# Kernel optimization log

Hardware: AMD Instinct MI355X
Metric: run time of the kernel (lower is better)

## Reference

```python
import jax, jax.numpy as jnp
import numpy as np

B, C, H8, W8 = 2, 256, 56, 96
RADIUS, LEVELS = 4, 4


def setup_inputs() -> dict:
    key = jax.random.key(0)
    k1, k2, k3, k4, k5 = jax.random.split(key, 5)
    fmap1 = jax.random.normal(k1, (B, C, H8, W8), jnp.float32)
    fmap2 = jax.random.normal(k2, (B, C, H8, W8), jnp.float32)
    xs = jnp.arange(W8, dtype=jnp.float32)
    ys = jnp.arange(H8, dtype=jnp.float32)
    bx, by = jnp.broadcast_arrays(xs[None, :], ys[:, None])
    base = jnp.stack([bx, by], axis=0)  # [2,H8,W8], x first (as create_coords_grid)
    coords = base[None] + 4.0 * jax.random.normal(k3, (B, 2, H8, W8), jnp.float32)
    flow = jax.random.normal(k4, (B, 2, H8, W8), jnp.float32)
    mask = jax.random.normal(k5, (B, 9 * 8 * 8, H8, W8), jnp.float32)
    return {"fmap1": fmap1, "fmap2": fmap2, "coords": coords, "flow": flow, "mask": mask}


def _bilinear_sample(cflat, Hl, Wl, px, py):
    # cflat: [N, Hl*Wl]; px,py: [N,P] pixel coords; zero padding outside (grid_sample default)
    x0 = jnp.floor(px)
    y0 = jnp.floor(py)
    wx = px - x0
    wy = py - y0
    x0 = x0.astype(jnp.int32)
    y0 = y0.astype(jnp.int32)

    def g(xi, yi):
        valid = (xi >= 0) & (xi <= Wl - 1) & (yi >= 0) & (yi <= Hl - 1)
        idx = jnp.clip(yi, 0, Hl - 1) * Wl + jnp.clip(xi, 0, Wl - 1)
        return jnp.where(valid, jnp.take_along_axis(cflat, idx, axis=1), 0.0)

    return ((1 - wy) * ((1 - wx) * g(x0, y0) + wx * g(x0 + 1, y0))
            + wy * ((1 - wx) * g(x0, y0 + 1) + wx * g(x0 + 1, y0 + 1)))


def _corr_lookup(fmap1, fmap2, coords):
    b, c, h, w = fmap1.shape
    n = b * h * w
    # all-pairs correlation, scaled by sqrt(C)
    corr = jnp.einsum('bchw,bcij->bhwij', fmap1, fmap2) / jnp.sqrt(jnp.float32(c))
    cl = corr.reshape(n, h, w)
    # query coords (pixel units at level 0)
    cx = coords[:, 0].reshape(n)
    cy = coords[:, 1].reshape(n)
    r = RADIUS
    lin = jnp.linspace(-r, r, 2 * r + 1, dtype=jnp.float32)
    # replicates torch.meshgrid(dy,dx) quirk: x-offset varies along axis 0, y along axis 1
    xo = jnp.repeat(lin, 2 * r + 1)  # [81]
    yo = jnp.tile(lin, 2 * r + 1)    # [81]
    outs = []
    for i in range(LEVELS):
        Hl, Wl = cl.shape[1], cl.shape[2]
        cflat = cl.reshape(n, Hl * Wl)
        px = cx[:, None] / (2 ** i) + xo[None, :]
        py = cy[:, None] / (2 ** i) + yo[None, :]
        samp = _bilinear_sample(cflat, Hl, Wl, px, py)  # [N,81]
        outs.append(samp.reshape(b, h, w, -1))
        if i < LEVELS - 1:  # 2x2 avg pool, stride 2
            cl = cl.reshape(n, Hl // 2, 2, Wl // 2, 2).mean(axis=(2, 4))
    out = jnp.concatenate(outs, axis=-1)  # [B,h,w,4*81]
    return out.transpose(0, 3, 1, 2)


def _convex_upsample(flow, mask):
    b, ch, h, w = flow.shape
    m = mask.reshape(b, 1, 9, 8, 8, h, w)
    m = jax.nn.softmax(m, axis=2)
    fp = jnp.pad(8.0 * flow, ((0, 0), (0, 0), (1, 1), (1, 1)))
    # 3x3 unfold, kernel positions row-major (matches F.unfold ordering)
    patches = jnp.stack([fp[:, :, i:i + h, j:j + w]
                         for i in range(3) for j in range(3)], axis=2)  # [B,2,9,h,w]
    up = jnp.sum(m * patches[:, :, :, None, None], axis=2)  # [B,2,8,8,h,w]
    up = up.transpose(0, 1, 4, 2, 5, 3)  # [B,2,h,8,w,8]
    return up.reshape(b, ch, 8 * h, 8 * w)


def reference(fmap1, fmap2, coords, flow, mask):
    corr_feats = _corr_lookup(fmap1, fmap2, coords)  # [B,324,H8,W8]
    up_flow = _convex_upsample(flow, mask)           # [B,2,8*H8,8*W8]
    return (corr_feats, up_flow)
```

## Files before the change

kernel.cpp:

```cpp
#include <hip/hip_runtime.h>
#include <math.h>

constexpr int B = 2, C = 256, H = 56, W = 96;
constexpr int HW = H * W;
constexpr int RADIUS = 4;

#define SQ 21.166666f
constexpr float SCL = 36.0f / (127.0f * 127.0f * 16.0f);

constexpr size_t F1T_B = 0;
constexpr size_t L0_B  = (size_t)B * HW * C;
constexpr size_t L1_B  = L0_B + (size_t)B * HW * C;
constexpr size_t L2_B  = L1_B + (size_t)B * 28 * 48 * C;
constexpr size_t L3_B  = L2_B + (size_t)B * 14 * 24 * C;
constexpr size_t OUT0_ELEMS = (size_t)B * 324 * HW;

static __device__ __forceinline__ int dot4acc(int a, int b, int c) {
#if __has_builtin(__builtin_amdgcn_sdot4)
    return __builtin_amdgcn_sdot4(a, b, c, false);
#else
    c += (int)(char)(a) * (int)(char)(b);
    c += (int)(char)(a >> 8) * (int)(char)(b >> 8);
    c += (int)(char)(a >> 16) * (int)(char)(b >> 16);
    c += (int)(char)(a >> 24) * (int)(char)(b >> 24);
    return c;
#endif
}

static __device__ __forceinline__ unsigned short pack_i8x2(float a, float b) {
    int ia = (int)rintf(a); ia = ia < -127 ? -127 : (ia > 127 ? 127 : ia);
    int ib = (int)rintf(b); ib = ib < -127 ? -127 : (ib > 127 ? 127 : ib);
    return (unsigned short)((ia & 0xFF) | ((ib & 0xFF) << 8));
}

constexpr int TP_BLOCKS = (HW / 32) * (C / 64) * 2 * B;
constexpr int CU_BLOCKS = B * H * 8;
constexpr int PL_BLOCKS = B * 7 * 12;
__global__ __launch_bounds__(256) void prep_kernel(
    const float* __restrict__ fmap1, const float* __restrict__ fmap2,
    const float* __restrict__ flow, const float* __restrict__ mask,
    char* __restrict__ ws, float* __restrict__ out1) {
    __shared__ float smem[72 * 96 + 2 * 3 * 98];
    int bid = blockIdx.x;
    int tid = threadIdx.x;

    if (bid < TP_BLOCKS) {
        float (*tile)[33] = (float(*)[33])smem;
        int zi = bid / 672;
        int rem = bid % 672;
        int by = rem / 168, bx = rem % 168;
        int b = zi & 1, m = zi >> 1;
        const float* src = m ? fmap2 : fmap1;
        unsigned short* dst = (unsigned short*)(ws + (m ? L0_B : F1T_B));
        int c0 = by * 64, q0 = bx * 32;
        int tx = tid & 31, ty = tid >> 5;
#pragma unroll
        for (int r = 0; r < 8; ++r) {
            int cl = ty + r * 8;
            tile[cl][tx] = src[((size_t)(b * C + c0 + cl)) * HW + q0 + tx];
        }
        __syncthreads();
#pragma unroll
        for (int r = 0; r < 4; ++r) {
            int pl = ty + r * 8;
            dst[((size_t)b * HW + q0 + pl) * 128 + (c0 >> 1) + tx] =
                pack_i8x2(tile[2 * tx][pl] * SQ, tile[2 * tx + 1][pl] * SQ);
        }
        return;
    }

    if (bid < TP_BLOCKS + CU_BLOCKS) {
        float* msk = smem;
        float* fst = smem + 72 * 96;
        int cb = bid - TP_BLOCKS;
        int i = cb & 7;
        int r = cb >> 3;
        int h = r % H;
        int b = r / H;

        for (int idx = tid; idx < 72 * 96; idx += 256) {
            int row = idx / 96, wc = idx - row * 96;
            int k = row >> 3, j = row & 7;
            int gl = k * 64 + i * 8 + j;
            msk[idx] = mask[((size_t)(b * 576 + gl)) * HW + h * W + wc];
        }
        for (int idx = tid; idx < 588; idx += 256) {
            int ch = idx / 294;
            int rem2 = idx - ch * 294;
            int rr = rem2 / 98;
            int xw = rem2 - rr * 98;
            int hh = h + rr - 1, ww = xw - 1;
            float v = 0.f;
            if (hh >= 0 && hh < H && ww >= 0 && ww < W)
                v = 8.0f * flow[((size_t)(b * 2 + ch)) * HW + hh * W + ww];
            fst[idx] = v;
        }
        __syncthreads();

#pragma unroll
        for (int rr = 0; rr < 3; ++rr) {
            int col = tid + rr * 256;
            int w = col >> 3, j = col & 7;
            float m[9], mx = -1e30f;
#pragma unroll
            for (int k = 0; k < 9; ++k) {
                m[k] = msk[(k * 8 + j) * 96 + w];
                mx = fmaxf(mx, m[k]);
            }
            float sum = 0.f;
#pragma unroll
            for (int k = 0; k < 9; ++k) {
                m[k] = __expf(m[k] - mx);
                sum += m[k];
            }
            float inv = 1.0f / sum;
            float a0 = 0.f, a1 = 0.f;
#pragma unroll
            for (int k = 0; k < 9; ++k) {
                int ki = k / 3, kj = k - ki * 3;
                float wgt = m[k] * inv;
                a0 = fmaf(wgt, fst[0 * 294 + ki * 98 + w + kj], a0);
                a1 = fmaf(wgt, fst[1 * 294 + ki * 98 + w + kj], a1);
            }
            size_t row8 = (size_t)8 * h + i;
            out1[((size_t)(b * 2 + 0) * 448 + row8) * 768 + col] = a0;
            out1[((size_t)(b * 2 + 1) * 448 + row8) * 768 + col] = a1;
        }
        return;
    }

    {
        int pb = bid - TP_BLOCKS - CU_BLOCKS;
        int b = pb / 84;
        int t = pb % 84;
        int y3 = t / 12, x3 = t % 12;
        int wv = tid >> 6, lane = tid & 63;
        int py = lane >> 3, px = lane & 7;

        unsigned short* D1 = (unsigned short*)(ws + L1_B);
        unsigned short* D2 = (unsigned short*)(ws + L2_B);
        unsigned short* D3 = (unsigned short*)(ws + L3_B);
        const float* srcp = fmap2 + (size_t)b * C * HW + (size_t)(y3 * 8 + py) * W + x3 * 8 + px;

        for (int j = wv * 32; j < wv * 32 + 32; ++j) {
            float va = srcp[(size_t)(2 * j) * HW];
            float vb = srcp[(size_t)(2 * j + 1) * HW];
            float a1 = va + __shfl_xor(va, 1); a1 += __shfl_xor(a1, 8);
            float b1 = vb + __shfl_xor(vb, 1); b1 += __shfl_xor(b1, 8);
            float a2 = a1 + __shfl_xor(a1, 2); a2 += __shfl_xor(a2, 16);
            float b2 = b1 + __shfl_xor(b1, 2); b2 += __shfl_xor(b2, 16);
            float a3 = a2 + __shfl_xor(a2, 4); a3 += __shfl_xor(a3, 32);
            float b3 = b2 + __shfl_xor(b2, 4); b3 += __shfl_xor(b3, 32);
            if ((lane & 9) == 0) {
                int Y = y3 * 4 + (py >> 1), X = x3 * 4 + (px >> 1);
                D1[((size_t)(b * 28 + Y) * 48 + X) * 128 + j] =
                    pack_i8x2(a1 * 0.25f * SQ, b1 * 0.25f * SQ);
            }
            if ((lane & 27) == 0) {
                int Y = y3 * 2 + (py >> 2), X = x3 * 2 + (px >> 2);
                D2[((size_t)(b * 14 + Y) * 24 + X) * 128 + j] =
                    pack_i8x2(a2 * 0.0625f * SQ, b2 * 0.0625f * SQ);
            }
            if (lane == 0) {
                D3[((size_t)(b * 7 + y3) * 12 + x3) * 128 + j] =
                    pack_i8x2(a3 * 0.015625f * SQ, b3 * 0.015625f * SQ);
            }
        }
    }
}

__global__ __launch_bounds__(256, 5) void corr_fused(
    const float* __restrict__ coords, const char* __restrict__ ws,
    float* __restrict__ out0) {
    __shared__ float Dsh[4][8][101];
    __shared__ float Wxy[4][8][2];

    int tid = threadIdx.x;
    int l = tid >> 6;
    int lane = tid & 63;
    int v = lane & 3;
    int grp = lane >> 2;

    int g0 = blockIdx.x * 8;
    int b = g0 / HW;
    int hw0 = g0 - b * HW;

    int Hl = H >> l, Wl = W >> l;
    size_t off = (l == 0 ? L0_B : (l == 1 ? L1_B : (l == 2 ? L2_B : L3_B)));
    const char* base8 = ws + off + (size_t)b * Hl * Wl * C;
    float scale = (l == 0 ? 1.0f : (l == 1 ? 0.5f : (l == 2 ? 0.25f : 0.125f)));

    int xo0 = grp < 10 ? grp : grp - 10;
    int yo0 = grp < 10 ? 0 : 1;

    const char* f1b = ws + F1T_B;

#pragma unroll 1
    for (int qi = 0; qi < 8; ++qi) {
        int g = g0 + qi;
        const int4* ap = (const int4*)(f1b + (size_t)g * C + (v << 6));
        int4 A0 = ap[0], A1 = ap[1], A2 = ap[2], A3 = ap[3];

        float cx = coords[(size_t)(b * 2 + 0) * HW + hw0 + qi];
        float cy = coords[(size_t)(b * 2 + 1) * HW + hw0 + qi];
        float fx = cx * scale, fy = cy * scale;
        float fxf = floorf(fx), fyf = floorf(fy);
        float wx = fx - fxf, wy = fy - fyf;
        int ix = (int)fxf, iy = (int)fyf;
        if (lane == 0) { Wxy[l][qi][0] = wx; Wxy[l][qi][1] = wy; }

        int xo = xo0, yo = yo0;
#pragma unroll
        for (int it = 0; it < 7; ++it) {
            bool live = (it < 6) | (grp < 4);
            int x = ix - RADIUS + xo;
            int y = iy - RADIUS + yo;
            int s0 = 0, s1 = 0, s2 = 0, s3 = 0;
            if (live && (unsigned)x < (unsigned)Wl && (unsigned)y < (unsigned)Hl) {
                const int4* cp = (const int4*)(base8 + ((y * Wl + x) << 8) + (v << 6));
                int4 c0 = cp[0], c1 = cp[1], c2 = cp[2], c3 = cp[3];
                s0 = dot4acc(c0.x, A0.x, s0); s1 = dot4acc(c0.y, A0.y, s1);
                s2 = dot4acc(c0.z, A0.z, s2); s3 = dot4acc(c0.w, A0.w, s3);
                s0 = dot4acc(c1.x, A1.x, s0); s1 = dot4acc(c1.y, A1.y, s1);
                s2 = dot4acc(c1.z, A1.z, s2); s3 = dot4acc(c1.w, A1.w, s3);
                s0 = dot4acc(c2.x, A2.x, s0); s1 = dot4acc(c2.y, A2.y, s1);
                s2 = dot4acc(c2.z, A2.z, s2); s3 = dot4acc(c2.w, A2.w, s3);
                s0 = dot4acc(c3.x, A3.x, s0); s1 = dot4acc(c3.y, A3.y, s1);
                s2 = dot4acc(c3.z, A3.z, s2); s3 = dot4acc(c3.w, A3.w, s3);
            }
            int s = (s0 + s1) + (s2 + s3);
            s += __shfl_xor(s, 1);
            s += __shfl_xor(s, 2);
            if (v == 0 && live) Dsh[l][qi][it * 16 + grp] = (float)s * SCL;
            xo += 6;
            int cr = xo >= 10;
            xo -= cr ? 10 : 0;
            yo += 1 + cr;
        }
    }
    __syncthreads();

    for (int o = tid; o < 324 * 8; o += 256) {
        int q = o & 7, ch = o >> 3;
        int lv = ch / 81;
        int o81 = ch - lv * 81;
        int xo = o81 / 9;
        int yo = o81 - xo * 9;
        float wxv = Wxy[lv][q][0], wyv = Wxy[lv][q][1];
        const float* D = Dsh[lv][q];
        float v00 = D[yo * 10 + xo];
        float v01 = D[yo * 10 + xo + 1];
        float v10 = D[yo * 10 + xo + 10];
        float v11 = D[yo * 10 + xo + 11];
        float res = (1.f - wyv) * ((1.f - wxv) * v00 + wxv * v01)
                  +        wyv  * ((1.f - wxv) * v10 + wxv * v11);
        out0[((size_t)(b * 324 + ch)) * HW + hw0 + q] = res;
    }
}

extern "C" void kernel_launch(void* const* d_in, const int* in_sizes, int n_in,
                              void* d_out, int out_size, void* d_ws, size_t ws_size,
                              hipStream_t stream) {
    const float* fmap1  = (const float*)d_in[0];
    const float* fmap2  = (const float*)d_in[1];
    const float* coords = (const float*)d_in[2];
    const float* flow   = (const float*)d_in[3];
    const float* maskp  = (const float*)d_in[4];
    float* out = (float*)d_out;
    char* ws = (char*)d_ws;

    prep_kernel<<<TP_BLOCKS + CU_BLOCKS + PL_BLOCKS, 256, 0, stream>>>(
        fmap1, fmap2, flow, maskp, ws, out + OUT0_ELEMS);
    corr_fused<<<B * HW / 8, 256, 0, stream>>>(coords, ws, out);
}
```

Measured before the change: 187.9 us.

## Compute correlation windows with int8 MFMA over per-block bounding boxes

Replaces the per-query sdot4 gather of 81 window dot products with a block that handles 16 queries at one pyramid level. It computes the union bounding box of their 10x10 windows and evaluates dense 16x16 int8 MFMA tiles over it, scattering hits into shared memory before bilinear interpolation. This moves the dot-product work onto matrix cores and shares each loaded fmap2 pixel across 16 queries. In exchange it computes extra correlations for box pixels outside any window, and the box grows when coordinates are spread out.

```diff
diff --git a/kernel.cpp b/kernel.cpp
--- a/kernel.cpp
+++ b/kernel.cpp
@@ -15,17 +15,8 @@
 constexpr size_t L3_B  = L2_B + (size_t)B * 14 * 24 * C;
 constexpr size_t OUT0_ELEMS = (size_t)B * 324 * HW;
 
-static __device__ __forceinline__ int dot4acc(int a, int b, int c) {
-#if __has_builtin(__builtin_amdgcn_sdot4)
-    return __builtin_amdgcn_sdot4(a, b, c, false);
-#else
-    c += (int)(char)(a) * (int)(char)(b);
-    c += (int)(char)(a >> 8) * (int)(char)(b >> 8);
-    c += (int)(char)(a >> 16) * (int)(char)(b >> 16);
-    c += (int)(char)(a >> 24) * (int)(char)(b >> 24);
-    return c;
-#endif
-}
+typedef int  v4i  __attribute__((ext_vector_type(4)));
+typedef long long ll2 __attribute__((ext_vector_type(2)));
 
 static __device__ __forceinline__ unsigned short pack_i8x2(float a, float b) {
     int ia = (int)rintf(a); ia = ia < -127 ? -127 : (ia > 127 ? 127 : ia);
@@ -169,92 +160,118 @@
     }
 }
 
-__global__ __launch_bounds__(256, 5) void corr_fused(
+__global__ __launch_bounds__(256, 4) void corr_mfma(
     const float* __restrict__ coords, const char* __restrict__ ws,
     float* __restrict__ out0) {
-    __shared__ float Dsh[4][8][101];
-    __shared__ float Wxy[4][8][2];
+    __shared__ int Dsh[16][101];
+    __shared__ float Wxy[16][2];
 
     int tid = threadIdx.x;
-    int l = tid >> 6;
+    int wave = tid >> 6;
     int lane = tid & 63;
-    int v = lane & 3;
-    int grp = lane >> 2;
-
-    int g0 = blockIdx.x * 8;
+    int q16 = lane & 15;
+    int m = lane >> 4;
+
+    int bid = blockIdx.x;
+    int l = bid & 3;
+    int qg = bid >> 2;
+    int g0 = qg * 16;
     int b = g0 / HW;
     int hw0 = g0 - b * HW;
+
+    int* dz = &Dsh[0][0];
+    for (int i = tid; i < 16 * 101; i += 256) dz[i] = 0;
 
     int Hl = H >> l, Wl = W >> l;
     size_t off = (l == 0 ? L0_B : (l == 1 ? L1_B : (l == 2 ? L2_B : L3_B)));
     const char* base8 = ws + off + (size_t)b * Hl * Wl * C;
     float scale = (l == 0 ? 1.0f : (l == 1 ? 0.5f : (l == 2 ? 0.25f : 0.125f)));
 
-    int xo0 = grp < 10 ? grp : grp - 10;
-    int yo0 = grp < 10 ? 0 : 1;
-
-    const char* f1b = ws + F1T_B;
-
-#pragma unroll 1
-    for (int qi = 0; qi < 8; ++qi) {
-        int g = g0 + qi;
-        const int4* ap = (const int4*)(f1b + (size_t)g * C + (v << 6));
-        int4 A0 = ap[0], A1 = ap[1], A2 = ap[2], A3 = ap[3];
-
-        float cx = coords[(size_t)(b * 2 + 0) * HW + hw0 + qi];
-        float cy = coords[(size_t)(b * 2 + 1) * HW + hw0 + qi];
-        float fx = cx * scale, fy = cy * scale;
-        float fxf = floorf(fx), fyf = floorf(fy);
-        float wx = fx - fxf, wy = fy - fyf;
-        int ix = (int)fxf, iy = (int)fyf;
-        if (lane == 0) { Wxy[l][qi][0] = wx; Wxy[l][qi][1] = wy; }
-
-        int xo = xo0, yo = yo0;
-#pragma unroll
-        for (int it = 0; it < 7; ++it) {
-            bool live = (it < 6) | (grp < 4);
-            int x = ix - RADIUS + xo;
-            int y = iy - RADIUS + yo;
-            int s0 = 0, s1 = 0, s2 = 0, s3 = 0;
-            if (live && (unsigned)x < (unsigned)Wl && (unsigned)y < (unsigned)Hl) {
-                const int4* cp = (const int4*)(base8 + ((y * Wl + x) << 8) + (v << 6));
-                int4 c0 = cp[0], c1 = cp[1], c2 = cp[2], c3 = cp[3];
-                s0 = dot4acc(c0.x, A0.x, s0); s1 = dot4acc(c0.y, A0.y, s1);
-                s2 = dot4acc(c0.z, A0.z, s2); s3 = dot4acc(c0.w, A0.w, s3);
-                s0 = dot4acc(c1.x, A1.x, s0); s1 = dot4acc(c1.y, A1.y, s1);
-                s2 = dot4acc(c1.z, A1.z, s2); s3 = dot4acc(c1.w, A1.w, s3);
-                s0 = dot4acc(c2.x, A2.x, s0); s1 = dot4acc(c2.y, A2.y, s1);
-                s2 = dot4acc(c2.z, A2.z, s2); s3 = dot4acc(c2.w, A2.w, s3);
-                s0 = dot4acc(c3.x, A3.x, s0); s1 = dot4acc(c3.y, A3.y, s1);
-                s2 = dot4acc(c3.z, A3.z, s2); s3 = dot4acc(c3.w, A3.w, s3);
-            }
-            int s = (s0 + s1) + (s2 + s3);
-            s += __shfl_xor(s, 1);
-            s += __shfl_xor(s, 2);
-            if (v == 0 && live) Dsh[l][qi][it * 16 + grp] = (float)s * SCL;
-            xo += 6;
-            int cr = xo >= 10;
-            xo -= cr ? 10 : 0;
-            yo += 1 + cr;
-        }
-    }
+    float cx = coords[(size_t)(b * 2 + 0) * HW + hw0 + q16];
+    float cy = coords[(size_t)(b * 2 + 1) * HW + hw0 + q16];
+    float fx = cx * scale, fy = cy * scale;
+    float fxf = floorf(fx), fyf = floorf(fy);
+    int ix = (int)fxf, iy = (int)fyf;
+    if (tid < 16) { Wxy[tid][0] = fx - fxf; Wxy[tid][1] = fy - fyf; }
+
+    int mnx = ix, mxx = ix, mny = iy, mxy = iy;
+#pragma unroll
+    for (int d = 1; d < 16; d <<= 1) {
+        mnx = min(mnx, __shfl_xor(mnx, d));
+        mxx = max(mxx, __shfl_xor(mxx, d));
+        mny = min(mny, __shfl_xor(mny, d));
+        mxy = max(mxy, __shfl_xor(mxy, d));
+    }
+    int bx0 = max(0, mnx - RADIUS), bx1 = min(Wl - 1, mxx + RADIUS + 1);
+    int by0 = max(0, mny - RADIUS), by1 = min(Hl - 1, mxy + RADIUS + 1);
+
+    int cxl = ix - RADIUS, cyl = iy - RADIUS;
+    int bq = m * 4;
+    int ax0 = __shfl(cxl, bq + 0), ay0 = __shfl(cyl, bq + 0);
+    int ax1 = __shfl(cxl, bq + 1), ay1 = __shfl(cyl, bq + 1);
+    int ax2 = __shfl(cxl, bq + 2), ay2 = __shfl(cyl, bq + 2);
+    int ax3 = __shfl(cxl, bq + 3), ay3 = __shfl(cyl, bq + 3);
+
+    const char* ab = ws + F1T_B + ((size_t)(g0 + q16)) * C + (m << 4);
+    ll2 A0 = *(const ll2*)(ab);
+    ll2 A1 = *(const ll2*)(ab + 64);
+    ll2 A2 = *(const ll2*)(ab + 128);
+    ll2 A3 = *(const ll2*)(ab + 192);
+
     __syncthreads();
 
-    for (int o = tid; o < 324 * 8; o += 256) {
-        int q = o & 7, ch = o >> 3;
-        int lv = ch / 81;
-        int o81 = ch - lv * 81;
-        int xo = o81 / 9;
-        int yo = o81 - xo * 9;
-        float wxv = Wxy[lv][q][0], wyv = Wxy[lv][q][1];
-        const float* D = Dsh[lv][q];
-        float v00 = D[yo * 10 + xo];
-        float v01 = D[yo * 10 + xo + 1];
-        float v10 = D[yo * 10 + xo + 10];
-        float v11 = D[yo * 10 + xo + 11];
+    for (int py = by0 + wave; py <= by1; py += 4) {
+        const char* rowb = base8 + (size_t)py * Wl * C + (m << 4);
+        for (int tx = bx0; tx <= bx1; tx += 16) {
+            int px = tx + q16;
+            bool pv = px <= bx1;
+            int pxc = pv ? px : bx1;
+            const char* pp = rowb + pxc * C;
+            ll2 B0 = *(const ll2*)(pp);
+            ll2 B1 = *(const ll2*)(pp + 64);
+            ll2 B2 = *(const ll2*)(pp + 128);
+            ll2 B3 = *(const ll2*)(pp + 192);
+            v4i acc0 = {0, 0, 0, 0}, acc1 = {0, 0, 0, 0};
+            acc0 = __builtin_amdgcn_mfma_i32_16x16x32_i8(A0.x, B0.x, acc0, 0, 0, 0);
+            acc0 = __builtin_amdgcn_mfma_i32_16x16x32_i8(A0.y, B0.y, acc0, 0, 0, 0);
+            acc0 = __builtin_amdgcn_mfma_i32_16x16x32_i8(A1.x, B1.x, acc0, 0, 0, 0);
+            acc0 = __builtin_amdgcn_mfma_i32_16x16x32_i8(A1.y, B1.y, acc0, 0, 0, 0);
+            acc1 = __builtin_amdgcn_mfma_i32_16x16x32_i8(A2.x, B2.x, acc1, 0, 0, 0);
+            acc1 = __builtin_amdgcn_mfma_i32_16x16x32_i8(A2.y, B2.y, acc1, 0, 0, 0);
+            acc1 = __builtin_amdgcn_mfma_i32_16x16x32_i8(A3.x, B3.x, acc1, 0, 0, 0);
+            acc1 = __builtin_amdgcn_mfma_i32_16x16x32_i8(A3.y, B3.y, acc1, 0, 0, 0);
+
+            int xo, yo;
+            xo = px - ax0; yo = py - ay0;
+            if (pv & ((unsigned)xo < 10u) & ((unsigned)yo < 10u))
+                Dsh[bq + 0][yo * 10 + xo] = acc0[0] + acc1[0];
+            xo = px - ax1; yo = py - ay1;
+            if (pv & ((unsigned)xo < 10u) & ((unsigned)yo < 10u))
+                Dsh[bq + 1][yo * 10 + xo] = acc0[1] + acc1[1];
+            xo = px - ax2; yo = py - ay2;
+            if (pv & ((unsigned)xo < 10u) & ((unsigned)yo < 10u))
+                Dsh[bq + 2][yo * 10 + xo] = acc0[2] + acc1[2];
+            xo = px - ax3; yo = py - ay3;
+            if (pv & ((unsigned)xo < 10u) & ((unsigned)yo < 10u))
+                Dsh[bq + 3][yo * 10 + xo] = acc0[3] + acc1[3];
+        }
+    }
+    __syncthreads();
+
+    int chbase = l * 81;
+    for (int o = tid; o < 81 * 16; o += 256) {
+        int q = o & 15, ch = o >> 4;
+        int xo = ch / 9;
+        int yo = ch - xo * 9;
+        float wxv = Wxy[q][0], wyv = Wxy[q][1];
+        const int* D = Dsh[q];
+        float v00 = (float)D[yo * 10 + xo] * SCL;
+        float v01 = (float)D[yo * 10 + xo + 1] * SCL;
+        float v10 = (float)D[yo * 10 + xo + 10] * SCL;
+        float v11 = (float)D[yo * 10 + xo + 11] * SCL;
         float res = (1.f - wyv) * ((1.f - wxv) * v00 + wxv * v01)
                   +        wyv  * ((1.f - wxv) * v10 + wxv * v11);
-        out0[((size_t)(b * 324 + ch)) * HW + hw0 + q] = res;
+        out0[((size_t)(b * 324 + chbase + ch)) * HW + hw0 + q] = res;
     }
 }
 
@@ -271,5 +288,5 @@
 
     prep_kernel<<<TP_BLOCKS + CU_BLOCKS + PL_BLOCKS, 256, 0, stream>>>(
         fmap1, fmap2, flow, maskp, ws, out + OUT0_ELEMS);
-    corr_fused<<<B * HW / 8, 256, 0, stream>>>(coords, ws, out);
-}
+    corr_mfma<<<4 * (B * HW / 16), 256, 0, stream>>>(coords, ws, out);
+}
```

After: 177.4 us. 5.6% less time.

## Move convex upsample into correlation kernel and regroup work per level

Applied to the files above, without the earlier changes.

Convex upsampling moves out of the prep kernel and into the main kernel. Its blocks are interleaved one-in-four with correlation blocks, so the mask-heavy work overlaps the correlation lookup instead of sitting in front of it. Correlation blocks now handle one pyramid level for 16 queries, with each wave taking 4 queries, rather than all four levels for 8 queries. The bounds checks before the int8 dot products become clamped, branch-free loads followed by masking. This shortens the dependent prep phase but raises shared-memory use per block and lowers the occupancy hint from 5 to 4.

```diff
diff --git a/kernel.cpp b/kernel.cpp
--- a/kernel.cpp
+++ b/kernel.cpp
@@ -34,18 +34,15 @@
 }
 
 constexpr int TP_BLOCKS = (HW / 32) * (C / 64) * 2 * B;
-constexpr int CU_BLOCKS = B * H * 8;
 constexpr int PL_BLOCKS = B * 7 * 12;
 __global__ __launch_bounds__(256) void prep_kernel(
     const float* __restrict__ fmap1, const float* __restrict__ fmap2,
-    const float* __restrict__ flow, const float* __restrict__ mask,
-    char* __restrict__ ws, float* __restrict__ out1) {
-    __shared__ float smem[72 * 96 + 2 * 3 * 98];
+    char* __restrict__ ws) {
+    __shared__ float tile[64][33];
     int bid = blockIdx.x;
     int tid = threadIdx.x;
 
     if (bid < TP_BLOCKS) {
-        float (*tile)[33] = (float(*)[33])smem;
         int zi = bid / 672;
         int rem = bid % 672;
         int by = rem / 168, bx = rem % 168;
@@ -69,68 +66,8 @@
         return;
     }
 
-    if (bid < TP_BLOCKS + CU_BLOCKS) {
-        float* msk = smem;
-        float* fst = smem + 72 * 96;
-        int cb = bid - TP_BLOCKS;
-        int i = cb & 7;
-        int r = cb >> 3;
-        int h = r % H;
-        int b = r / H;
-
-        for (int idx = tid; idx < 72 * 96; idx += 256) {
-            int row = idx / 96, wc = idx - row * 96;
-            int k = row >> 3, j = row & 7;
-            int gl = k * 64 + i * 8 + j;
-            msk[idx] = mask[((size_t)(b * 576 + gl)) * HW + h * W + wc];
-        }
-        for (int idx = tid; idx < 588; idx += 256) {
-            int ch = idx / 294;
-            int rem2 = idx - ch * 294;
-            int rr = rem2 / 98;
-            int xw = rem2 - rr * 98;
-            int hh = h + rr - 1, ww = xw - 1;
-            float v = 0.f;
-            if (hh >= 0 && hh < H && ww >= 0 && ww < W)
-                v = 8.0f * flow[((size_t)(b * 2 + ch)) * HW + hh * W + ww];
-            fst[idx] = v;
-        }
-        __syncthreads();
-
-#pragma unroll
-        for (int rr = 0; rr < 3; ++rr) {
-            int col = tid + rr * 256;
-            int w = col >> 3, j = col & 7;
-            float m[9], mx = -1e30f;
-#pragma unroll
-            for (int k = 0; k < 9; ++k) {
-                m[k] = msk[(k * 8 + j) * 96 + w];
-                mx = fmaxf(mx, m[k]);
-            }
-            float sum = 0.f;
-#pragma unroll
-            for (int k = 0; k < 9; ++k) {
-                m[k] = __expf(m[k] - mx);
-                sum += m[k];
-            }
-            float inv = 1.0f / sum;
-            float a0 = 0.f, a1 = 0.f;
-#pragma unroll
-            for (int k = 0; k < 9; ++k) {
-                int ki = k / 3, kj = k - ki * 3;
-                float wgt = m[k] * inv;
-                a0 = fmaf(wgt, fst[0 * 294 + ki * 98 + w + kj], a0);
-                a1 = fmaf(wgt, fst[1 * 294 + ki * 98 + w + kj], a1);
-            }
-            size_t row8 = (size_t)8 * h + i;
-            out1[((size_t)(b * 2 + 0) * 448 + row8) * 768 + col] = a0;
-            out1[((size_t)(b * 2 + 1) * 448 + row8) * 768 + col] = a1;
-        }
-        return;
-    }
-
     {
-        int pb = bid - TP_BLOCKS - CU_BLOCKS;
+        int pb = bid - TP_BLOCKS;
         int b = pb / 84;
         int t = pb % 84;
         int y3 = t / 12, x3 = t % 12;
@@ -169,56 +106,76 @@
     }
 }
 
-__global__ __launch_bounds__(256, 5) void corr_fused(
+constexpr int NCORR = 2688;
+constexpr int NCONV = B * H * 8;
+__global__ __launch_bounds__(256, 4) void main_kernel(
     const float* __restrict__ coords, const char* __restrict__ ws,
-    float* __restrict__ out0) {
-    __shared__ float Dsh[4][8][101];
-    __shared__ float Wxy[4][8][2];
-
+    const float* __restrict__ flow, const float* __restrict__ mask,
+    float* __restrict__ out0, float* __restrict__ out1) {
+    __shared__ float smem[72 * 96 + 2 * 3 * 98];
+    int bid = blockIdx.x;
     int tid = threadIdx.x;
-    int l = tid >> 6;
-    int lane = tid & 63;
-    int v = lane & 3;
-    int grp = lane >> 2;
-
-    int g0 = blockIdx.x * 8;
-    int b = g0 / HW;
-    int hw0 = g0 - b * HW;
-
-    int Hl = H >> l, Wl = W >> l;
-    size_t off = (l == 0 ? L0_B : (l == 1 ? L1_B : (l == 2 ? L2_B : L3_B)));
-    const char* base8 = ws + off + (size_t)b * Hl * Wl * C;
-    float scale = (l == 0 ? 1.0f : (l == 1 ? 0.5f : (l == 2 ? 0.25f : 0.125f)));
-
-    int xo0 = grp < 10 ? grp : grp - 10;
-    int yo0 = grp < 10 ? 0 : 1;
-
-    const char* f1b = ws + F1T_B;
+    int gq = bid >> 2, sel = bid & 3;
+
+    if (sel < 3) {
+        int cid = gq * 3 + sel;
+        float (*Dsh)[101] = (float(*)[101])smem;
+        float (*Wxy)[2]   = (float(*)[2])(smem + 16 * 101);
+
+        int wave = tid >> 6;
+        int lane = tid & 63;
+        int v = lane & 3;
+        int grp = lane >> 2;
+
+        int l = cid & 3;
+        int qg = cid >> 2;
+        int g0 = qg * 16;
+        int b = g0 / HW;
+        int hw0 = g0 - b * HW;
+
+        int Hl = H >> l, Wl = W >> l;
+        int Wlm1 = Wl - 1, Hlm1 = Hl - 1;
+        size_t off = (l == 0 ? L0_B : (l == 1 ? L1_B : (l == 2 ? L2_B : L3_B)));
+        const char* base8 = ws + off + (size_t)b * Hl * Wl * C;
+        float scale = (l == 0 ? 1.0f : (l == 1 ? 0.5f : (l == 2 ? 0.25f : 0.125f)));
+
+        int xo0 = grp < 10 ? grp : grp - 10;
+        int yo0 = grp < 10 ? 0 : 1;
+
+        const char* f1b = ws + F1T_B;
 
 #pragma unroll 1
-    for (int qi = 0; qi < 8; ++qi) {
-        int g = g0 + qi;
-        const int4* ap = (const int4*)(f1b + (size_t)g * C + (v << 6));
-        int4 A0 = ap[0], A1 = ap[1], A2 = ap[2], A3 = ap[3];
-
-        float cx = coords[(size_t)(b * 2 + 0) * HW + hw0 + qi];
-        float cy = coords[(size_t)(b * 2 + 1) * HW + hw0 + qi];
-        float fx = cx * scale, fy = cy * scale;
-        float fxf = floorf(fx), fyf = floorf(fy);
-        float wx = fx - fxf, wy = fy - fyf;
-        int ix = (int)fxf, iy = (int)fyf;
-        if (lane == 0) { Wxy[l][qi][0] = wx; Wxy[l][qi][1] = wy; }
-
-        int xo = xo0, yo = yo0;
-#pragma unroll
-        for (int it = 0; it < 7; ++it) {
-            bool live = (it < 6) | (grp < 4);
-            int x = ix - RADIUS + xo;
-            int y = iy - RADIUS + yo;
-            int s0 = 0, s1 = 0, s2 = 0, s3 = 0;
-            if (live && (unsigned)x < (unsigned)Wl && (unsigned)y < (unsigned)Hl) {
-                const int4* cp = (const int4*)(base8 + ((y * Wl + x) << 8) + (v << 6));
-                int4 c0 = cp[0], c1 = cp[1], c2 = cp[2], c3 = cp[3];
+        for (int qi = 0; qi < 4; ++qi) {
+            int wq = wave * 4 + qi;
+            int g = g0 + wq;
+            const char* ab = f1b + (size_t)g * C + (v << 4);
+            int4 A0 = *(const int4*)(ab);
+            int4 A1 = *(const int4*)(ab + 64);
+            int4 A2 = *(const int4*)(ab + 128);
+            int4 A3 = *(const int4*)(ab + 192);
+
+            float cx = coords[(size_t)(b * 2 + 0) * HW + hw0 + wq];
+            float cy = coords[(size_t)(b * 2 + 1) * HW + hw0 + wq];
+            float fx = cx * scale, fy = cy * scale;
+            float fxf = floorf(fx), fyf = floorf(fy);
+            float wx = fx - fxf, wy = fy - fyf;
+            int ix = (int)fxf, iy = (int)fyf;
+            if (lane == 0) { Wxy[wq][0] = wx; Wxy[wq][1] = wy; }
+
+            int xo = xo0, yo = yo0;
+#pragma unroll
+            for (int it = 0; it < 7; ++it) {
+                int x = ix - RADIUS + xo;
+                int y = iy - RADIUS + yo;
+                bool valid = ((unsigned)x < (unsigned)Wl) & ((unsigned)y < (unsigned)Hl);
+                int xc = min(max(x, 0), Wlm1);
+                int yc = min(max(y, 0), Hlm1);
+                const char* rp = base8 + ((yc * Wl + xc) << 8) + (v << 4);
+                int4 c0 = *(const int4*)(rp);
+                int4 c1 = *(const int4*)(rp + 64);
+                int4 c2 = *(const int4*)(rp + 128);
+                int4 c3 = *(const int4*)(rp + 192);
+                int s0 = 0, s1 = 0, s2 = 0, s3 = 0;
                 s0 = dot4acc(c0.x, A0.x, s0); s1 = dot4acc(c0.y, A0.y, s1);
                 s2 = dot4acc(c0.z, A0.z, s2); s3 = dot4acc(c0.w, A0.w, s3);
                 s0 = dot4acc(c1.x, A1.x, s0); s1 = dot4acc(c1.y, A1.y, s1);
@@ -227,34 +184,93 @@
                 s2 = dot4acc(c2.z, A2.z, s2); s3 = dot4acc(c2.w, A2.w, s3);
                 s0 = dot4acc(c3.x, A3.x, s0); s1 = dot4acc(c3.y, A3.y, s1);
                 s2 = dot4acc(c3.z, A3.z, s2); s3 = dot4acc(c3.w, A3.w, s3);
-            }
-            int s = (s0 + s1) + (s2 + s3);
-            s += __shfl_xor(s, 1);
-            s += __shfl_xor(s, 2);
-            if (v == 0 && live) Dsh[l][qi][it * 16 + grp] = (float)s * SCL;
-            xo += 6;
-            int cr = xo >= 10;
-            xo -= cr ? 10 : 0;
-            yo += 1 + cr;
-        }
+                int s = (s0 + s1) + (s2 + s3);
+                s = valid ? s : 0;
+                s += __shfl_xor(s, 1);
+                s += __shfl_xor(s, 2);
+                bool live = (it < 6) | (grp < 4);
+                if (v == 0 && live) Dsh[wq][it * 16 + grp] = (float)s * SCL;
+                xo += 6;
+                int cr = xo >= 10;
+                xo -= cr ? 10 : 0;
+                yo += 1 + cr;
+            }
+        }
+        __syncthreads();
+
+        int chbase = l * 81;
+        for (int o = tid; o < 81 * 16; o += 256) {
+            int q = o & 15, ch = o >> 4;
+            int xo = ch / 9;
+            int yo = ch - xo * 9;
+            float wxv = Wxy[q][0], wyv = Wxy[q][1];
+            const float* D = Dsh[q];
+            float v00 = D[yo * 10 + xo];
+            float v01 = D[yo * 10 + xo + 1];
+            float v10 = D[yo * 10 + xo + 10];
+            float v11 = D[yo * 10 + xo + 11];
+            float res = (1.f - wyv) * ((1.f - wxv) * v00 + wxv * v01)
+                      +        wyv  * ((1.f - wxv) * v10 + wxv * v11);
+            out0[((size_t)(b * 324 + chbase + ch)) * HW + hw0 + q] = res;
+        }
+        return;
+    }
+
+    float* msk = smem;
+    float* fst = smem + 72 * 96;
+    int cb = gq;
+    int i = cb & 7;
+    int r = cb >> 3;
+    int h = r % H;
+    int b = r / H;
+
+    for (int idx = tid; idx < 72 * 96; idx += 256) {
+        int row = idx / 96, wc = idx - row * 96;
+        int k = row >> 3, j = row & 7;
+        int gl = k * 64 + i * 8 + j;
+        msk[idx] = mask[((size_t)(b * 576 + gl)) * HW + h * W + wc];
+    }
+    for (int idx = tid; idx < 588; idx += 256) {
+        int ch = idx / 294;
+        int rem2 = idx - ch * 294;
+        int rr = rem2 / 98;
+        int xw = rem2 - rr * 98;
+        int hh = h + rr - 1, ww = xw - 1;
+        float v = 0.f;
+        if (hh >= 0 && hh < H && ww >= 0 && ww < W)
+            v = 8.0f * flow[((size_t)(b * 2 + ch)) * HW + hh * W + ww];
+        fst[idx] = v;
     }
     __syncthreads();
 
-    for (int o = tid; o < 324 * 8; o += 256) {
-        int q = o & 7, ch = o >> 3;
-        int lv = ch / 81;
-        int o81 = ch - lv * 81;
-        int xo = o81 / 9;
-        int yo = o81 - xo * 9;
-        float wxv = Wxy[lv][q][0], wyv = Wxy[lv][q][1];
-        const float* D = Dsh[lv][q];
-        float v00 = D[yo * 10 + xo];
-        float v01 = D[yo * 10 + xo + 1];
-        float v10 = D[yo * 10 + xo + 10];
-        float v11 = D[yo * 10 + xo + 11];
-        float res = (1.f - wyv) * ((1.f - wxv) * v00 + wxv * v01)
-                  +        wyv  * ((1.f - wxv) * v10 + wxv * v11);
-        out0[((size_t)(b * 324 + ch)) * HW + hw0 + q] = res;
+#pragma unroll
+    for (int rr = 0; rr < 3; ++rr) {
+        int col = tid + rr * 256;
+        int w = col >> 3, j = col & 7;
+        float m[9], mx = -1e30f;
+#pragma unroll
+        for (int k = 0; k < 9; ++k) {
+            m[k] = msk[(k * 8 + j) * 96 + w];
+            mx = fmaxf(mx, m[k]);
+        }
+        float sum = 0.f;
+#pragma unroll
+        for (int k = 0; k < 9; ++k) {
+            m[k] = __expf(m[k] - mx);
+            sum += m[k];
+        }
+        float inv = 1.0f / sum;
+        float a0 = 0.f, a1 = 0.f;
+#pragma unroll
+        for (int k = 0; k < 9; ++k) {
+            int ki = k / 3, kj = k - ki * 3;
+            float wgt = m[k] * inv;
+            a0 = fmaf(wgt, fst[0 * 294 + ki * 98 + w + kj], a0);
+            a1 = fmaf(wgt, fst[1 * 294 + ki * 98 + w + kj], a1);
+        }
+        size_t row8 = (size_t)8 * h + i;
+        out1[((size_t)(b * 2 + 0) * 448 + row8) * 768 + col] = a0;
+        out1[((size_t)(b * 2 + 1) * 448 + row8) * 768 + col] = a1;
     }
 }
 
@@ -269,7 +285,7 @@
     float* out = (float*)d_out;
     char* ws = (char*)d_ws;
 
-    prep_kernel<<<TP_BLOCKS + CU_BLOCKS + PL_BLOCKS, 256, 0, stream>>>(
-        fmap1, fmap2, flow, maskp, ws, out + OUT0_ELEMS);
-    corr_fused<<<B * HW / 8, 256, 0, stream>>>(coords, ws, out);
-}
+    prep_kernel<<<TP_BLOCKS + PL_BLOCKS, 256, 0, stream>>>(fmap1, fmap2, ws);
+    main_kernel<<<4 * NCONV, 256, 0, stream>>>(coords, ws, flow, maskp,
+                                               out, out + OUT0_ELEMS);
+}
```

Result: faster. 169.0 us (-10.1%).
